# Kernel optimization log

Hardware: AMD Instinct MI355X
Metric: run time of the kernel (lower is better)

The kernel has to match this reference:

```python
import jax, jax.numpy as jnp
import numpy as np

EPS = 1e-4
SILU_GAIN = 1.0 / 0.596  # magnitude-preserving SiLU gain
SCALES = (4, 4, 8)       # prod == A_DIM == 128
T = 0.3                  # residual lerp weight


def mp_silu(x):
    return jax.nn.silu(x) * SILU_GAIN


def pixel_norm(x):
    # normalize over channel dim (axis=1) to unit RMS
    return x * jax.lax.rsqrt(jnp.mean(jnp.square(x), axis=1, keepdims=True) + EPS)


def norm_w(w):
    # magnitude-preserving conv: per-output-filter L2-normalized weight
    n = jnp.sqrt(jnp.sum(jnp.square(w), axis=tuple(range(1, w.ndim)), keepdims=True) + 1e-8)
    return w / n


def mp_add(a, b, t=T):
    return (a * (1.0 - t) + b * t) / np.sqrt((1.0 - t) ** 2 + t ** 2)


def conv2d(x, w, groups=1, padding=((0, 0), (0, 0))):
    return jax.lax.conv_general_dilated(
        x, w, (1, 1), padding,
        dimension_numbers=('NCHW', 'OIHW', 'NCHW'), feature_group_count=groups)


def conv1d(x, w, groups=1, padding=((0, 0),)):
    return jax.lax.conv_general_dilated(
        x, w, (1,), padding,
        dimension_numbers=('NCH', 'OIH', 'NCH'), feature_group_count=groups)


def avgpool_freq(x, s):
    B, C, F, L = x.shape
    return jnp.mean(x.reshape(B, C, F // s, s, L), axis=3)


def min_gru(h, w):
    # minGRU: z_t = sigmoid(Wz h_t), c_t = Wc h_t, s_t = (1-z_t) s_{t-1} + z_t c_t
    z, c = jnp.split(conv1d(h, norm_w(w)), 2, axis=1)
    z = jax.nn.sigmoid(z)
    a, b = 1.0 - z, z * c  # linear recurrence s_t = a_t s_{t-1} + b_t

    def comb(x, y):
        a1, b1 = x
        a2, b2 = y
        return a2 * a1, a2 * b1 + b2

    _, out = jax.lax.associative_scan(comb, (a, b), axis=-1)
    return out


def conv_block(x, w1, wd, w2, wdn, s):
    # x: [B, d, F, L]
    x = pixel_norm(x)
    r = mp_silu(x)
    r = conv2d(r, norm_w(w1))                                            # d -> h, 1x1
    r = conv2d(r, norm_w(wd), groups=wd.shape[0], padding=((2, 2), (1, 1)))  # depthwise 5x3
    r = mp_silu(r)
    r = conv2d(r, norm_w(w2))                                            # h -> d, 1x1
    h = mp_add(x, r)
    return conv2d(avgpool_freq(h, s), norm_w(wdn))                       # d -> 2d, freq /s


def seq_block(x, hg_w, dw_w, gru_w, out_w):
    # x: [B, d, L]
    x = pixel_norm(x)
    h, g = jnp.split(conv1d(x, norm_w(hg_w)), 2, axis=1)  # each [B, H, L]
    h = mp_silu(h)
    h = conv1d(h, norm_w(dw_w), groups=dw_w.shape[0], padding=((1, 1),))  # depthwise k=3
    h = mp_silu(h)
    h = min_gru(h, gru_w)
    h = h * mp_silu(g)
    return mp_add(x, conv1d(h, norm_w(out_w)))


def setup_inputs() -> dict:
    key = jax.random.key(0)
    ks = jax.random.split(key, 18)
    rn = lambda k, s: jax.random.normal(k, s, dtype=jnp.float32)
    B, L, A = 2, 2048, 128
    return {
        'audio': rn(ks[0], (B, A, L)),
        'proj_w': rn(ks[1], (64, 1, 1, 1)) * 0.5,
        'proj_b': jnp.zeros((64,), jnp.float32),
        'c0_w1': rn(ks[2], (128, 64, 1, 1)),
        'c0_wd': rn(ks[3], (128, 1, 5, 3)),
        'c0_w2': rn(ks[4], (64, 128, 1, 1)),
        'c0_dn': rn(ks[5], (128, 64, 1, 1)),
        'c1_w1': rn(ks[6], (256, 128, 1, 1)),
        'c1_wd': rn(ks[7], (256, 1, 5, 3)),
        'c1_w2': rn(ks[8], (128, 256, 1, 1)),
        'c1_dn': rn(ks[9], (256, 128, 1, 1)),
        'c2_w1': rn(ks[10], (512, 256, 1, 1)),
        'c2_wd': rn(ks[11], (512, 1, 5, 3)),
        'c2_w2': rn(ks[12], (256, 512, 1, 1)),
        'c2_dn': rn(ks[13], (512, 256, 1, 1)),
        'hg_w': rn(ks[14], (4, 2048, 512, 1)),
        'dw_w': rn(ks[15], (4, 1024, 1, 3)),
        'gru_w': rn(ks[16], (4, 2048, 1024, 1)),
        'out_w': rn(ks[17], (4, 512, 1024, 1)),
    }


def reference(audio, proj_w, proj_b,
              c0_w1, c0_wd, c0_w2, c0_dn,
              c1_w1, c1_wd, c1_w2, c1_dn,
              c2_w1, c2_wd, c2_w2, c2_dn,
              hg_w, dw_w, gru_w, out_w):
    h = audio[:, None]  # [B, 1, A_DIM, L]
    h = conv2d(h, proj_w) + proj_b[None, :, None, None]
    blocks = ((c0_w1, c0_wd, c0_w2, c0_dn),
              (c1_w1, c1_wd, c1_w2, c1_dn),
              (c2_w1, c2_wd, c2_w2, c2_dn))
    for (w1, wd, w2, dn), s in zip(blocks, SCALES):
        h = conv_block(h, w1, wd, w2, dn, s)
    h = h[:, :, 0, :]  # freq dim reduced to 1 -> [B, dim, L]
    for i in range(hg_w.shape[0]):
        h = seq_block(h, hg_w[i], dw_w[i], gru_w[i], out_w[i])
    return mp_silu(h)
```

## Files before the change

### kernel.cpp

```cpp
#include <hip/hip_runtime.h>
#include <math.h>

#define GAIN 1.6778523489932886f
#define MPS  1.3130643285972254f

typedef __attribute__((ext_vector_type(8))) short short8;
typedef __attribute__((ext_vector_type(4))) short short4v;
typedef __attribute__((ext_vector_type(4))) float float4v;

__device__ __forceinline__ float silu_g(float x){
  float s = 1.0f/(1.0f + __expf(-x));
  return x*s*GAIN;
}
__device__ __forceinline__ short f2bf(float f){
  unsigned u = __builtin_bit_cast(unsigned, f);
  u += 0x7fffu + ((u >> 16) & 1u);
  return (short)(u >> 16);
}
__device__ __forceinline__ float bf2f(unsigned short h){
  return __builtin_bit_cast(float, ((unsigned)h) << 16);
}

typedef __attribute__((address_space(3))) unsigned int as3_uint;
typedef const __attribute__((address_space(1))) unsigned int as1_cuint;
__device__ __forceinline__ void gload16(const unsigned short* gsrc, unsigned short* ldst){
  __builtin_amdgcn_global_load_lds((as1_cuint*)gsrc, (as3_uint*)ldst, 16, 0, 0);
}

struct NcEnt { const float* w; int O, K, dstOff; };
struct NcArgs { NcEnt e[16]; };

__global__ __launch_bounds__(64) void normcast_kernel(NcArgs na, unsigned short* __restrict__ wbf){
  int row = blockIdx.x;
  int base = 0; int i;
  for (i = 0; i < 16; i++){
    if (row < base + na.e[i].O) break;
    base += na.e[i].O;
  }
  if (i >= 16) return;
  int r = row - base; int K = na.e[i].K;
  const float* w = na.e[i].w + (long)r*K;
  unsigned short* dst = wbf + na.e[i].dstOff + (long)r*K;
  int tid = threadIdx.x;
  float s = 0.f;
  const bool v4 = ((K & 3) == 0);
  if (v4){
    for (int k = tid*4; k < K; k += 256){
      float4v v = *(const float4v*)&w[k];
      s += v[0]*v[0] + v[1]*v[1] + v[2]*v[2] + v[3]*v[3];
    }
  } else {
    for (int k = tid; k < K; k += 64){ float v = w[k]; s += v*v; }
  }
  for (int off = 32; off; off >>= 1) s += __shfl_down(s, off);
  float inv = rsqrtf(__shfl(s, 0) + 1e-8f);
  if (v4){
    for (int k = tid*4; k < K; k += 256){
      float4v v = *(const float4v*)&w[k];
      short4v o = { f2bf(v[0]*inv), f2bf(v[1]*inv), f2bf(v[2]*inv), f2bf(v[3]*inv) };
      *(short4v*)&dst[k] = o;
    }
  } else {
    for (int k = tid; k < K; k += 64) dst[k] = (unsigned short)f2bf(w[k]*inv);
  }
}

__global__ __launch_bounds__(64) void projstats_kernel(const float* __restrict__ pw, const float* __restrict__ pb,
                                                       float* __restrict__ S){
  int t = threadIdx.x;
  float p = pw[t], q = pb[t];
  float s1 = p*p, s2 = p*q, s3 = q*q;
  for (int off = 32; off; off >>= 1){
    s1 += __shfl_down(s1, off); s2 += __shfl_down(s2, off); s3 += __shfl_down(s3, off);
  }
  if (t == 0){ S[0] = s1; S[1] = s2; S[2] = s3; }
}

__global__ __launch_bounds__(256) void invn_audio_kernel(const float* __restrict__ audio, const float* __restrict__ S,
                                                         float* __restrict__ invn){
  long i = blockIdx.x*256 + threadIdx.x;
  if (i >= (2L*128*2048)/4) return;
  long e = i*4;
  float S1 = S[0], S2 = S[1], S3 = S[2];
  float4v a = *(const float4v*)&audio[e];
  float4v o;
  #pragma unroll
  for (int j = 0; j < 4; j++) o[j] = rsqrtf((a[j]*a[j]*S1 + 2.f*a[j]*S2 + S3)/64.f + 1e-4f);
  *(float4v*)&invn[e] = o;
}

template<int G, bool BF>
__global__ __launch_bounds__(256) void invn_reduce_kernel(const void* __restrict__ Xv, float* __restrict__ invn,
                                                          int C, int F){
  constexpr int L = 256/G;
  int t = threadIdx.x; int cs = t / L; int li = t % L;
  long pos = (long)blockIdx.x*L + li;
  int bf = (int)(pos >> 11); int l = (int)(pos & 2047);
  int b = bf / F; int f = bf - b*F;
  long base = ((long)b*C*F + f)*2048 + l;
  long stride = (long)F*2048;
  float s = 0.f;
  if (BF){
    const unsigned short* X = (const unsigned short*)Xv;
    for (int c = cs; c < C; c += G){ float v = bf2f(X[base + (long)c*stride]); s += v*v; }
  } else {
    const float* X = (const float*)Xv;
    for (int c = cs; c < C; c += G){ float v = X[base + (long)c*stride]; s += v*v; }
  }
  __shared__ float red[256];
  red[t] = s; __syncthreads();
  #pragma unroll
  for (int off = G/2; off > 0; off >>= 1){
    if (cs < off) red[t] += red[t + off*L];
    __syncthreads();
  }
  if (cs == 0) invn[pos] = rsqrtf(red[li]/(float)C + 1e-4f);
}

template<bool SILU, bool BF>
__global__ __launch_bounds__(256) void applynorm_kernel(const void* __restrict__ Xv, const float* __restrict__ invn,
                                                        unsigned short* __restrict__ XB, int C, int F, long total4){
  long i = blockIdx.x*256 + threadIdx.x;
  if (i >= total4) return;
  long e = i*4;
  int l = (int)(e & 2047); long r = e >> 11;
  int f = (int)(r % F); long bc = r / F; int b = (int)(bc / C);
  float4v x;
  if (BF){
    short4v u = *(const short4v*)((const unsigned short*)Xv + e);
    x = (float4v){ bf2f((unsigned short)u[0]), bf2f((unsigned short)u[1]),
                   bf2f((unsigned short)u[2]), bf2f((unsigned short)u[3]) };
  } else {
    x = *(const float4v*)((const float*)Xv + e);
  }
  float4v iv = *(const float4v*)&invn[((long)b*F + f)*2048 + l];
  short4v o;
  #pragma unroll
  for (int j = 0; j < 4; j++){
    float v = x[j]*iv[j];
    o[j] = f2bf(SILU ? silu_g(v) : v);
  }
  *(short4v*)&XB[e] = o;
}

__global__ __launch_bounds__(256) void normT_kernel(const float* __restrict__ SEQ,
                                                    const float* __restrict__ invn,
                                                    unsigned short* __restrict__ XST){
  __shared__ float tile[64][65];
  const int l0 = blockIdx.x*64, c0 = blockIdx.y*64, b = blockIdx.z;
  const int t = threadIdx.x;
  const int lr = (t & 15)*4;
  const int cr = t >> 4;
  #pragma unroll
  for (int p = 0; p < 4; p++){
    int c = cr + p*16;
    float4v v = *(const float4v*)&SEQ[((long)(b*512 + c0 + c))*2048 + l0 + lr];
    tile[c][lr+0] = v[0]; tile[c][lr+1] = v[1]; tile[c][lr+2] = v[2]; tile[c][lr+3] = v[3];
  }
  __syncthreads();
  const int cc = (t & 7)*8;
  const int lw = t >> 3;
  #pragma unroll
  for (int p = 0; p < 2; p++){
    int l = lw + p*32;
    float iv = invn[b*2048 + l0 + l];
    short8 o;
    #pragma unroll
    for (int j = 0; j < 8; j++) o[j] = f2bf(tile[cc+j][l] * iv);
    *(short8*)&XST[((long)(b*2048 + l0 + l))*512 + c0 + cc] = o;
  }
}

struct GTArgs {
  const unsigned short* A;
  const unsigned short* B;
  unsigned short* O1;
  unsigned short* O2;
  int N, K;
};

template<int EMODE>
__global__ __launch_bounds__(256,2) void gemmT_kernel(GTArgs g){
  __shared__ __align__(16) char SMEMraw[49152];
  unsigned short (*Asm)[4096] = (unsigned short (*)[4096])SMEMraw;
  unsigned short (*Bsm)[4096] = (unsigned short (*)[4096])(SMEMraw + 24576);
  const int t = threadIdx.x;
  const int lane = t & 63;
  const int wc = (t >> 7) & 1;
  const int wsd = (t >> 6) & 1;
  const int q = lane >> 4, r16 = lane & 15;
  const int m0 = blockIdx.x * 128;
  const int n0 = blockIdx.y * 128;
  const int K = g.K;

  const int r0 = t >> 2;
  const int c8 = (((t & 3) ^ ((r0 >> 1) & 3)) << 3);
  const unsigned short* Ap = g.A + (long)(n0 + r0)*K + c8;
  const unsigned short* Bp = g.B + (long)(m0 + r0)*K + c8;

  auto stage = [&](int bi, int k0){
    gload16(Ap + k0,           &Asm[bi][t*8]);
    gload16(Ap + 64*K + k0,    &Asm[bi][2048 + t*8]);
    gload16(Bp + k0,           &Bsm[bi][t*8]);
    gload16(Bp + 64*K + k0,    &Bsm[bi][2048 + t*8]);
  };

  float4v acc[4][4];
  #pragma unroll
  for (int i = 0; i < 4; i++)
    #pragma unroll
    for (int j = 0; j < 4; j++) acc[i][j] = (float4v){0.f,0.f,0.f,0.f};

  const int nit = K >> 5;
  stage(0, 0);
  stage(1, 32);

  const int qsw = ((q ^ ((r16 >> 1) & 3)) << 3);

  for (int it = 0; it < nit; ++it){
    if (it + 2 < nit){
      stage((it + 2) % 3, (it + 2) << 5);
      asm volatile("" ::: "memory");
      asm volatile("s_waitcnt vmcnt(8)" ::: "memory");
    } else if (it + 1 < nit){
      asm volatile("s_waitcnt vmcnt(4)" ::: "memory");
    } else {
      asm volatile("s_waitcnt vmcnt(0)" ::: "memory");
    }
    __builtin_amdgcn_s_barrier();
    asm volatile("" ::: "memory");

    const unsigned short* As = Asm[it % 3];
    const unsigned short* Bs = Bsm[it % 3];
    short8 afr[4], bfr[4];
    #pragma unroll
    for (int i = 0; i < 4; i++) afr[i] = *(const short8*)&As[(wc*64 + i*16 + r16)*32 + qsw];
    #pragma unroll
    for (int j = 0; j < 4; j++) bfr[j] = *(const short8*)&Bs[(wsd*64 + j*16 + r16)*32 + qsw];
    #pragma unroll
    for (int i = 0; i < 4; i++)
      #pragma unroll
      for (int j = 0; j < 4; j++)
        acc[i][j] = __builtin_amdgcn_mfma_f32_16x16x32_bf16(afr[i], bfr[j], acc[i][j], 0, 0, 0);

    asm volatile("" ::: "memory");
    __builtin_amdgcn_s_barrier();
  }

  if (EMODE == 1 && n0 < 1024){
    float* Cf = (float*)SMEMraw;
    #pragma unroll
    for (int h = 0; h < 2; h++){
      __syncthreads();
      if (wc == h){
        #pragma unroll
        for (int j = 0; j < 4; j++){
          int m = wsd*64 + j*16 + r16;
          #pragma unroll
          for (int i = 0; i < 4; i++)
            *(float4v*)&Cf[m*68 + i*16 + q*4] = acc[i][j];
        }
      }
      __syncthreads();
      #pragma unroll
      for (int p = 0; p < 4; p++){
        int m = (t >> 3) + p*32;
        int n8 = (t & 7)*8;
        int gm = m0 + m; int b = gm >> 11, l = gm & 2047;
        float4v v0 = *(const float4v*)&Cf[m*68 + n8];
        float4v v1 = *(const float4v*)&Cf[m*68 + n8 + 4];
        short8 o;
        #pragma unroll
        for (int e = 0; e < 4; e++){ o[e] = f2bf(silu_g(v0[e])); o[e+4] = f2bf(silu_g(v1[e])); }
        *(short8*)&g.O1[((long)(b*2048 + l))*1024 + (n0 + h*64 + n8)] = o;
      }
    }
  } else {
    float* Csm = (float*)SMEMraw;
    #pragma unroll
    for (int qtr = 0; qtr < 4; qtr++){
      __syncthreads();
      if (wc == (qtr >> 1)){
        #pragma unroll
        for (int ii = 0; ii < 2; ii++){
          int i = (qtr & 1)*2 + ii;
          #pragma unroll
          for (int j = 0; j < 4; j++){
            int m = wsd*64 + j*16 + r16;
            #pragma unroll
            for (int rg = 0; rg < 4; rg++)
              Csm[(ii*16 + q*4 + rg)*132 + m] = acc[i][j][rg];
          }
        }
      }
      __syncthreads();
      #pragma unroll
      for (int sp = 0; sp < 2; sp++){
        int nrow = (t >> 4) + sp*16;
        int n = n0 + qtr*32 + nrow;
        int m8 = (t & 15)*8;
        int gm = m0 + m8; int b = gm >> 11, l = gm & 2047;
        float4v v0 = *(const float4v*)&Csm[nrow*132 + m8];
        float4v v1 = *(const float4v*)&Csm[nrow*132 + m8 + 4];
        short8 o;
        #pragma unroll
        for (int e = 0; e < 4; e++){ o[e] = f2bf(v0[e]); o[e+4] = f2bf(v1[e]); }
        if (EMODE == 1) *(short8*)&g.O2[((long)(b*1024 + (n - 1024)))*2048 + l] = o;
        else            *(short8*)&g.O1[((long)(b*2048 + n))*2048 + l] = o;
      }
    }
  }
}

struct GemmArgs {
  const unsigned short* A;
  const unsigned short* Bh;
  const float* invn; const float* audio;
  const float* pw; const float* pb;
  const unsigned short* auxXH;
  unsigned short* CoutH; unsigned short* Cout2H;
  int N, K, Fdim, Lw, lq0, BLw, Bl0, CLw, Cl0, Nsto, Fsrc;
};

template<int BMODE, int EMODE>
__global__ __launch_bounds__(256,2) void mgemm_kernel(GemmArgs g){
  __shared__ __align__(16) char SMEMraw[20480];
  unsigned short* Asm = (unsigned short*)SMEMraw;
  unsigned short* Bsm = Asm + 128*40;
  const int t = threadIdx.x;
  const int lane = t & 63;
  const int wave = t >> 6;
  const int wc = wave >> 1, wsd = wave & 1;
  const int q = lane >> 4, r16 = lane & 15;
  const int s0 = blockIdx.x * 128;
  const int n0 = blockIdx.y * 128;
  const int FL = g.Fdim * g.Lw;

  const int ar = t >> 1, ah = t & 1;
  const int an = n0 + ar;
  const bool aval = an < g.N;
  const unsigned short* Aptr = g.A + (long)an*g.K + ah*16;

  const int kg = t & 7, mg = t >> 3;
  const int mb = s0 + mg*4;
  int bcol = mb / FL; int rr = mb - bcol*FL;
  int fcol = (g.Fdim > 1) ? (rr / g.Lw) : 0;
  int labs = g.lq0 + (rr - fcol*g.Lw);
  const bool cv = (bcol < 2);
  bool lv[4];
  #pragma unroll
  for (int j = 0; j < 4; j++) lv[j] = cv && (labs + j >= 0) && (labs + j < 2048);
  const bool vec4 = cv && (labs >= 0) && (labs + 3 < 2048);
  const unsigned short* bbase = g.Bh;
  if (cv) bbase = g.Bh + ((long)(bcol*g.K)*g.Fsrc + fcol)*g.BLw + (labs - g.Bl0);
  const long kstep = (long)g.Fsrc * g.BLw;

  float invn4[4] = {0,0,0,0}, aud4[4] = {0,0,0,0};
  if (BMODE == 2){
    #pragma unroll
    for (int j = 0; j < 4; j++) if (lv[j]){
      invn4[j] = g.invn[(bcol*g.Fdim + fcol)*2048 + labs + j];
      aud4[j]  = g.audio[(bcol*128 + fcol)*2048 + labs + j];
    }
  }

  float4v acc[4][4];
  #pragma unroll
  for (int i = 0; i < 4; i++)
    #pragma unroll
    for (int j = 0; j < 4; j++) acc[i][j] = (float4v){0.f,0.f,0.f,0.f};

  short8 pa0 = {0,0,0,0,0,0,0,0}, pa1 = {0,0,0,0,0,0,0,0};
  short4v praw[4];
  #pragma unroll
  for (int i = 0; i < 4; i++) praw[i] = (short4v){0,0,0,0};

  auto ldA = [&](int kb){
    if (aval){
      pa0 = *(const short8*)(Aptr + kb);
      pa1 = *(const short8*)(Aptr + kb + 8);
    }
  };
  auto ldB = [&](int kb){
    #pragma unroll
    for (int i = 0; i < 4; i++){
      const int k = kb + kg*4 + i;
      const unsigned short* bp = bbase + (long)k*kstep;
      if (vec4) praw[i] = *(const short4v*)bp;
      else {
        short4v u = {0,0,0,0};
        #pragma unroll
        for (int j = 0; j < 4; j++) if (lv[j]) u[j] = (short)bp[j];
        praw[i] = u;
      }
    }
  };

  ldA(0);
  if (BMODE == 0) ldB(0);

  for (int k0 = 0; k0 < g.K; k0 += 32){
    short8 sa0 = pa0, sa1 = pa1;
    short4v bpk[4];
    if (BMODE == 0){
      #pragma unroll
      for (int j = 0; j < 4; j++){
        short4v p;
        #pragma unroll
        for (int i = 0; i < 4; i++) p[i] = praw[i][j];
        bpk[j] = p;
      }
    } else {
      float tv[4][4];
      #pragma unroll
      for (int i = 0; i < 4; i++){
        const int k = k0 + kg*4 + i;
        const float pwk = g.pw[k], pbk = g.pb[k];
        #pragma unroll
        for (int j = 0; j < 4; j++) tv[i][j] = lv[j] ? silu_g((aud4[j]*pwk + pbk)*invn4[j]) : 0.f;
      }
      #pragma unroll
      for (int j = 0; j < 4; j++){
        short4v p;
        #pragma unroll
        for (int i = 0; i < 4; i++) p[i] = f2bf(tv[i][j]);
        bpk[j] = p;
      }
    }
    if (k0 + 32 < g.K){
      ldA(k0 + 32);
      if (BMODE == 0) ldB(k0 + 32);
    }

    __syncthreads();
    *(short8*)&Asm[ar*40 + ah*16]     = sa0;
    *(short8*)&Asm[ar*40 + ah*16 + 8] = sa1;
    #pragma unroll
    for (int j = 0; j < 4; j++)
      *(short4v*)&Bsm[(mg*4 + j)*40 + kg*4] = bpk[j];
    __syncthreads();

    short8 afr[4], bfr[4];
    #pragma unroll
    for (int i = 0; i < 4; i++) afr[i] = *(const short8*)&Asm[(wc*64 + i*16 + r16)*40 + q*8];
    #pragma unroll
    for (int j = 0; j < 4; j++) bfr[j] = *(const short8*)&Bsm[(wsd*64 + j*16 + r16)*40 + q*8];
    #pragma unroll
    for (int i = 0; i < 4; i++)
      #pragma unroll
      for (int j = 0; j < 4; j++)
        acc[i][j] = __builtin_amdgcn_mfma_f32_16x16x32_bf16(afr[i], bfr[j], acc[i][j], 0, 0, 0);
  }

  {
    float* Csm = (float*)SMEMraw;
    #pragma unroll
    for (int qtr = 0; qtr < 4; qtr++){
      __syncthreads();
      if (wc == (qtr >> 1)){
        #pragma unroll
        for (int ii = 0; ii < 2; ii++){
          int i = (qtr & 1)*2 + ii;
          #pragma unroll
          for (int j = 0; j < 4; j++){
            int m = wsd*64 + j*16 + r16;
            #pragma unroll
            for (int rg = 0; rg < 4; rg++)
              Csm[(ii*16 + q*4 + rg)*132 + m] = acc[i][j][rg];
          }
        }
      }
      __syncthreads();
      #pragma unroll
      for (int sp = 0; sp < 2; sp++){
        int nrow = (t >> 4) + sp*16;
        int n = n0 + qtr*32 + nrow;
        int m8 = (t & 15)*8;
        if (n >= g.N) continue;
        int sg = s0 + m8;
        int b2 = sg / FL; int r2 = sg - b2*FL;
        if (b2 >= 2) continue;
        int f2 = (g.Fdim > 1) ? (r2 / g.Lw) : 0;
        int l2 = g.lq0 + (r2 - f2*g.Lw);
        float4v v0 = *(const float4v*)&Csm[nrow*132 + m8];
        float4v v1 = *(const float4v*)&Csm[nrow*132 + m8 + 4];
        long obase = ((long)(b2*g.Nsto + n)*g.Fdim + f2)*g.CLw + (l2 - g.Cl0);
        short8 o;
        if (EMODE == 1){
          #pragma unroll
          for (int e = 0; e < 4; e++){ o[e] = f2bf(v0[e]); o[e+4] = f2bf(v1[e]); }
        } else if (EMODE == 2){
          short8 axv = *(const short8*)&g.auxXH[((long)(b2*g.N + n)*g.Fdim + f2)*2048 + l2];
          const float* ivp = &g.invn[(b2*g.Fdim + f2)*2048 + l2];
          float4v iv0 = *(const float4v*)ivp;
          float4v iv1 = *(const float4v*)(ivp + 4);
          #pragma unroll
          for (int e = 0; e < 4; e++){
            float xn0 = bf2f((unsigned short)axv[e]) * iv0[e];
            float xn1 = bf2f((unsigned short)axv[e+4]) * iv1[e];
            o[e]   = f2bf((xn0*0.7f + v0[e]*0.3f)*MPS);
            o[e+4] = f2bf((xn1*0.7f + v1[e]*0.3f)*MPS);
          }
        } else {
          float pwn = g.pw[n], pbn = g.pb[n];
          const float* ap  = &g.audio[(b2*128 + f2)*2048 + l2];
          const float* ivp = &g.invn[(b2*g.Fdim + f2)*2048 + l2];
          float4v a0 = *(const float4v*)ap,  a1 = *(const float4v*)(ap + 4);
          float4v iv0 = *(const float4v*)ivp, iv1 = *(const float4v*)(ivp + 4);
          #pragma unroll
          for (int e = 0; e < 4; e++){
            float xn0 = (a0[e]*pwn + pbn)*iv0[e];
            float xn1 = (a1[e]*pwn + pbn)*iv1[e];
            o[e]   = f2bf((xn0*0.7f + v0[e]*0.3f)*MPS);
            o[e+4] = f2bf((xn1*0.7f + v1[e]*0.3f)*MPS);
          }
        }
        *(short8*)&g.CoutH[obase] = o;
      }
    }
  }
}

struct DnArgs {
  const unsigned short* A; const unsigned short* P;
  float* Cout; unsigned short* CoutH;
  int N, K, F2, Lc, l0;
};

template<int EMODE>
__global__ __launch_bounds__(256,4) void mgemm64_kernel(DnArgs g){
  __shared__ __align__(16) char SMEM[10240];
  unsigned short* Asm = (unsigned short*)SMEM;
  unsigned short* Bsm = Asm + 64*40;
  const int t = threadIdx.x;
  const int lane = t & 63;
  const int wave = t >> 6;
  const int wc = wave >> 1, wsd = wave & 1;
  const int q = lane >> 4, r16 = lane & 15;
  const int s0 = blockIdx.x * 64;
  const int n0 = blockIdx.y * 64;
  const int FL = g.F2 * g.Lc;

  const int ar = t >> 2, ah = t & 3;
  const unsigned short* Aptr = g.A + (long)(n0 + ar)*g.K + ah*8;
  const int kg = t & 7, mg = t >> 3;
  const bool bstage = (mg < 16);
  const int mb = s0 + (mg & 15)*4;
  const int bcol = mb / FL; const int rr = mb - bcol*FL;
  const int fcol = rr / g.Lc; const int li = rr - fcol*g.Lc;
  const unsigned short* bbase = g.P + ((long)(bcol*g.K)*g.F2 + fcol)*g.Lc + li;
  const long kstep = (long)g.F2 * g.Lc;

  float4v acc[2][2];
  #pragma unroll
  for (int i = 0; i < 2; i++)
    #pragma unroll
    for (int j = 0; j < 2; j++) acc[i][j] = (float4v){0.f,0.f,0.f,0.f};

  short8 pa = {0,0,0,0,0,0,0,0};
  short4v praw[4];
  #pragma unroll
  for (int i = 0; i < 4; i++) praw[i] = (short4v){0,0,0,0};

  auto ldA = [&](int kb){ pa = *(const short8*)(Aptr + kb); };
  auto ldB = [&](int kb){
    if (bstage){
      #pragma unroll
      for (int i = 0; i < 4; i++)
        praw[i] = *(const short4v*)(bbase + (long)(kb + kg*4 + i)*kstep);
    }
  };
  ldA(0); ldB(0);

  for (int k0 = 0; k0 < g.K; k0 += 32){
    short8 sa = pa;
    short4v bpk[4];
    #pragma unroll
    for (int j = 0; j < 4; j++){
      short4v p;
      #pragma unroll
      for (int i = 0; i < 4; i++) p[i] = praw[i][j];
      bpk[j] = p;
    }
    if (k0 + 32 < g.K){ ldA(k0 + 32); ldB(k0 + 32); }

    __syncthreads();
    *(short8*)&Asm[ar*40 + ah*8] = sa;
    if (bstage){
      #pragma unroll
      for (int j = 0; j < 4; j++)
        *(short4v*)&Bsm[((mg & 15)*4 + j)*40 + kg*4] = bpk[j];
    }
    __syncthreads();

    short8 afr[2], bfr[2];
    #pragma unroll
    for (int i = 0; i < 2; i++) afr[i] = *(const short8*)&Asm[(wc*32 + i*16 + r16)*40 + q*8];
    #pragma unroll
    for (int j = 0; j < 2; j++) bfr[j] = *(const short8*)&Bsm[(wsd*32 + j*16 + r16)*40 + q*8];
    #pragma unroll
    for (int i = 0; i < 2; i++)
      #pragma unroll
      for (int j = 0; j < 2; j++)
        acc[i][j] = __builtin_amdgcn_mfma_f32_16x16x32_bf16(afr[i], bfr[j], acc[i][j], 0, 0, 0);
  }

  {
    float* Csm = (float*)SMEM;
    const int b2 = s0 / FL; const int r20 = s0 - b2*FL;
    const int f2c = r20 / g.Lc; const int l2c = g.l0 + (r20 - f2c*g.Lc);
    #pragma unroll
    for (int nq = 0; nq < 4; nq++){
      __syncthreads();
      if (wc == (nq >> 1)){
        const int i = nq & 1;
        #pragma unroll
        for (int j = 0; j < 2; j++)
          #pragma unroll
          for (int rg = 0; rg < 4; rg++)
            Csm[(q*4 + rg)*68 + wsd*32 + j*16 + r16] = acc[i][j][rg];
      }
      __syncthreads();
      int nrow = t >> 4;
      int mq = (t & 15)*4;
      int n = n0 + nq*16 + nrow;
      float4v v = *(const float4v*)&Csm[nrow*68 + mq];
      long oidx = ((long)(b2*g.N + n)*g.F2 + f2c)*2048 + l2c + mq;
      if (EMODE == 0){
        *(float4v*)&g.Cout[oidx] = v;
      } else {
        short4v o = { f2bf(v[0]), f2bf(v[1]), f2bf(v[2]), f2bf(v[3]) };
        *(short4v*)&g.CoutH[oidx] = o;
      }
    }
  }
}

template<int EMODE>
__global__ __launch_bounds__(256,4) void seqout_kernel(const unsigned short* __restrict__ A,
                                                       const unsigned short* __restrict__ Bh,
                                                       const float* __restrict__ invn,
                                                       const float* __restrict__ auxX,
                                                       float* __restrict__ Cout, int K){
  __shared__ __align__(16) char SMEM[10240];
  unsigned short* Asm = (unsigned short*)SMEM;
  unsigned short* Bsm = Asm + 64*40;
  const int t = threadIdx.x;
  const int lane = t & 63;
  const int wave = t >> 6;
  const int wc = wave >> 1, wsd = wave & 1;
  const int q = lane >> 4, r16 = lane & 15;
  const int s0 = blockIdx.x * 64;
  const int n0 = blockIdx.y * 64;

  const int ar = t >> 2, ah = t & 3;
  const unsigned short* Aptr = A + (long)(n0 + ar)*K + ah*8;
  const int kg = t & 7, mg = t >> 3;
  const bool bstage = (mg < 16);
  const int mb = s0 + (mg & 15)*4;
  const int bcol = mb >> 11, lb = mb & 2047;
  const unsigned short* bbase = Bh + ((long)bcol*K)*2048 + lb;

  float4v acc[2][2];
  #pragma unroll
  for (int i = 0; i < 2; i++)
    #pragma unroll
    for (int j = 0; j < 2; j++) acc[i][j] = (float4v){0.f,0.f,0.f,0.f};

  short8 pa = {0,0,0,0,0,0,0,0};
  short4v praw[4];
  #pragma unroll
  for (int i = 0; i < 4; i++) praw[i] = (short4v){0,0,0,0};

  auto ldA = [&](int kb){ pa = *(const short8*)(Aptr + kb); };
  auto ldB = [&](int kb){
    if (bstage){
      #pragma unroll
      for (int i = 0; i < 4; i++)
        praw[i] = *(const short4v*)(bbase + (long)(kb + kg*4 + i)*2048);
    }
  };
  ldA(0); ldB(0);

  for (int k0 = 0; k0 < K; k0 += 32){
    short8 sa = pa;
    short4v bpk[4];
    #pragma unroll
    for (int j = 0; j < 4; j++){
      short4v p;
      #pragma unroll
      for (int i = 0; i < 4; i++) p[i] = praw[i][j];
      bpk[j] = p;
    }
    if (k0 + 32 < K){ ldA(k0 + 32); ldB(k0 + 32); }

    __syncthreads();
    *(short8*)&Asm[ar*40 + ah*8] = sa;
    if (bstage){
      #pragma unroll
      for (int j = 0; j < 4; j++)
        *(short4v*)&Bsm[((mg & 15)*4 + j)*40 + kg*4] = bpk[j];
    }
    __syncthreads();

    short8 afr[2], bfr[2];
    #pragma unroll
    for (int i = 0; i < 2; i++) afr[i] = *(const short8*)&Asm[(wc*32 + i*16 + r16)*40 + q*8];
    #pragma unroll
    for (int j = 0; j < 2; j++) bfr[j] = *(const short8*)&Bsm[(wsd*32 + j*16 + r16)*40 + q*8];
    #pragma unroll
    for (int i = 0; i < 2; i++)
      #pragma unroll
      for (int j = 0; j < 2; j++)
        acc[i][j] = __builtin_amdgcn_mfma_f32_16x16x32_bf16(afr[i], bfr[j], acc[i][j], 0, 0, 0);
  }

  {
    float* Csm = (float*)SMEM;
    const int b2 = s0 >> 11; const int l0b = s0 & 2047;
    #pragma unroll
    for (int nq = 0; nq < 4; nq++){
      __syncthreads();
      if (wc == (nq >> 1)){
        const int i = nq & 1;
        #pragma unroll
        for (int j = 0; j < 2; j++)
          #pragma unroll
          for (int rg = 0; rg < 4; rg++)
            Csm[(q*4 + rg)*68 + wsd*32 + j*16 + r16] = acc[i][j][rg];
      }
      __syncthreads();
      int nrow = t >> 4;
      int mq = (t & 15)*4;
      int n = n0 + nq*16 + nrow;
      int l = l0b + mq;
      float4v v = *(const float4v*)&Csm[nrow*68 + mq];
      float4v ax = *(const float4v*)&auxX[((long)b2*512 + n)*2048 + l];
      float4v iv = *(const float4v*)&invn[b2*2048 + l];
      float4v r;
      #pragma unroll
      for (int e = 0; e < 4; e++){
        float xn = ax[e]*iv[e];
        float rr = (xn*0.7f + v[e]*0.3f)*MPS;
        r[e] = (EMODE == 6) ? silu_g(rr) : rr;
      }
      *(float4v*)&Cout[((long)b2*512 + n)*2048 + l] = r;
    }
  }
}

__global__ __launch_bounds__(256) void poolf_kernel(const unsigned short* __restrict__ Hb,
                                                    unsigned short* __restrict__ P,
                                                    int F2, int s, int Lc, long total4){
  long i = blockIdx.x*256 + threadIdx.x;
  if (i >= total4) return;
  long e = i*4;
  int li = (int)(e % Lc); long r0 = e / Lc;
  int f2 = (int)(r0 % F2); long r = r0 / F2;
  const unsigned short* src = Hb + ((long)r*F2*s + (long)f2*s)*Lc + li;
  float a0=0,a1=0,a2=0,a3=0;
  for (int p = 0; p < s; p++){
    short4v u = *(const short4v*)(src + (long)p*Lc);
    a0 += bf2f((unsigned short)u[0]); a1 += bf2f((unsigned short)u[1]);
    a2 += bf2f((unsigned short)u[2]); a3 += bf2f((unsigned short)u[3]);
  }
  float inv = 1.f/(float)s;
  short4v o = { f2bf(a0*inv), f2bf(a1*inv), f2bf(a2*inv), f2bf(a3*inv) };
  *(short4v*)&P[((long)r*F2 + f2)*Lc + li] = o;
}

struct DwArgs { const unsigned short* R1; const unsigned short* wd; unsigned short* R2; int C, F, Lc, l0; };
__global__ __launch_bounds__(256) void dw2d_kernel(DwArgs a){
  int idx = blockIdx.x*256 + threadIdx.x;
  int Lq = a.Lc >> 3;
  int Fq = a.F >> 3;
  int total = 2*a.C*Fq*Lq;
  if (idx >= total) return;
  int lq = idx % Lq; int r = idx / Lq;
  int fq = r % Fq; r /= Fq;
  int c = r % a.C; int b = r / a.C;
  int f0 = fq*8;
  int labs = a.l0 + lq*8;
  int Lw = a.Lc + 8;
  const unsigned short* base = a.R1 + (long)((b*a.C + c)*a.F)*Lw + (labs - (a.l0 - 4));
  const unsigned short* w = a.wd + c*15;
  float W[5][3];
  #pragma unroll
  for (int tp = 0; tp < 5; tp++)
    #pragma unroll
    for (int j = 0; j < 3; j++) W[tp][j] = bf2f(w[tp*3 + j]);

  const bool llo = (labs > 0);
  const bool lhi = (labs + 8 < 2048);
  float acc[8][8];
  #pragma unroll
  for (int t = 0; t < 8; t++)
    #pragma unroll
    for (int j = 0; j < 8; j++) acc[t][j] = 0.f;

  #pragma unroll
  for (int r12 = 0; r12 < 12; r12++){
    int rrow = f0 - 2 + r12;
    if (rrow < 0 || rrow >= a.F) continue;
    const unsigned short* p = base + (long)rrow*Lw;
    short4v u0 = *(const short4v*)p;
    short4v u1 = *(const short4v*)(p + 4);
    float x[10];
    x[0] = llo ? bf2f(p[-1]) : 0.f;
    x[1] = bf2f((unsigned short)u0[0]); x[2] = bf2f((unsigned short)u0[1]);
    x[3] = bf2f((unsigned short)u0[2]); x[4] = bf2f((unsigned short)u0[3]);
    x[5] = bf2f((unsigned short)u1[0]); x[6] = bf2f((unsigned short)u1[1]);
    x[7] = bf2f((unsigned short)u1[2]); x[8] = bf2f((unsigned short)u1[3]);
    x[9] = lhi ? bf2f(p[8]) : 0.f;
    #pragma unroll
    for (int t = 0; t < 8; t++){
      const int df = r12 - 2 - t;
      if (df < -2 || df > 2) continue;
      float w0 = W[df+2][0], w1 = W[df+2][1], w2 = W[df+2][2];
      #pragma unroll
      for (int j = 0; j < 8; j++)
        acc[t][j] += w0*x[j] + w1*x[j+1] + w2*x[j+2];
    }
  }

  unsigned short* ob = a.R2 + ((long)((b*a.C + c)*a.F + f0))*a.Lc + (labs - a.l0);
  #pragma unroll
  for (int t = 0; t < 8; t++){
    short8 o;
    #pragma unroll
    for (int j = 0; j < 8; j++) o[j] = f2bf(silu_g(acc[t][j]));
    *(short8*)(ob + (long)t*a.Lc) = o;
  }
}

__global__ __launch_bounds__(256) void dwseqT_kernel(const unsigned short* __restrict__ HST,
                                                     const unsigned short* __restrict__ w,
                                                     unsigned short* __restrict__ H2T){
  int idx = blockIdx.x*256 + threadIdx.x;
  if (idx >= 2*2048*128) return;
  int c0 = (idx & 127) * 8; long bt = idx >> 7;
  int tt = (int)(bt & 2047);
  const unsigned short* base = HST + bt*1024 + c0;
  short8 zz = {0,0,0,0,0,0,0,0};
  short8 x1 = *(const short8*)base;
  short8 x0 = (tt > 0)    ? *(const short8*)(base - 1024) : zz;
  short8 x2 = (tt < 2047) ? *(const short8*)(base + 1024) : zz;
  const unsigned short* wp = w + c0*3;
  short8 o;
  #pragma unroll
  for (int j = 0; j < 8; j++){
    float w0 = bf2f(wp[3*j]), w1 = bf2f(wp[3*j+1]), w2 = bf2f(wp[3*j+2]);
    float v = w0*bf2f((unsigned short)x0[j]) + w1*bf2f((unsigned short)x1[j]) + w2*bf2f((unsigned short)x2[j]);
    o[j] = f2bf(silu_g(v));
  }
  *(short8*)&H2T[bt*1024 + c0] = o;
}

__global__ __launch_bounds__(256) void scan_kernel(const unsigned short* __restrict__ ZC, const unsigned short* __restrict__ G,
                                                   unsigned short* __restrict__ SC){
  int bc = blockIdx.x;
  int b = bc >> 10, c = bc & 1023;
  const unsigned short* zrow = ZC + ((long)(b*2048 + c))*2048;
  const unsigned short* crow = ZC + ((long)(b*2048 + 1024 + c))*2048;
  const unsigned short* grow = G + (long)bc*2048;
  unsigned short* orow = SC + (long)bc*2048;
  int tid = threadIdx.x;
  int t0 = tid*8;
  short8 zv = *(const short8*)&zrow[t0];
  short8 cv = *(const short8*)&crow[t0];
  float av[8], bv[8];
  float A = 1.f, Bv = 0.f;
  #pragma unroll
  for (int j = 0; j < 8; j++){
    float z = bf2f((unsigned short)zv[j]); float cval = bf2f((unsigned short)cv[j]);
    float zs = 1.f/(1.f + __expf(-z));
    float a = 1.f - zs; float bb = zs*cval;
    av[j] = a; bv[j] = bb;
    Bv = a*Bv + bb;
    A = a*A;
  }
  __shared__ float sA[256], sB[256];
  sA[tid] = A; sB[tid] = Bv;
  __syncthreads();
  for (int off = 1; off < 256; off <<= 1){
    float pA = 1.f, pB = 0.f;
    if (tid >= off){ pA = sA[tid-off]; pB = sB[tid-off]; }
    __syncthreads();
    float nA = A*pA; float nB = A*pB + Bv;
    A = nA; Bv = nB;
    sA[tid] = A; sB[tid] = Bv;
    __syncthreads();
  }
  float h = (tid > 0) ? sB[tid-1] : 0.f;
  short8 gv = *(const short8*)&grow[t0];
  short8 ov;
  #pragma unroll
  for (int j = 0; j < 8; j++){
    h = av[j]*h + bv[j];
    ov[j] = f2bf(h * silu_g(bf2f((unsigned short)gv[j])));
  }
  *(short8*)&orow[t0] = ov;
}

extern "C" void kernel_launch(void* const* d_in, const int* in_sizes, int n_in,
                              void* d_out, int out_size, void* d_ws, size_t ws_size,
                              hipStream_t stream) {
  const float* audio = (const float*)d_in[0];
  const float* pw = (const float*)d_in[1];
  const float* pb = (const float*)d_in[2];
  const float* cw1[3] = {(const float*)d_in[3], (const float*)d_in[7], (const float*)d_in[11]};
  const float* cwd[3] = {(const float*)d_in[4], (const float*)d_in[8], (const float*)d_in[12]};
  const float* cw2[3] = {(const float*)d_in[5], (const float*)d_in[9], (const float*)d_in[13]};
  const float* cdn[3] = {(const float*)d_in[6], (const float*)d_in[10], (const float*)d_in[14]};
  const float* hgw  = (const float*)d_in[15];
  const float* dww  = (const float*)d_in[16];
  const float* gruw = (const float*)d_in[17];
  const float* outw = (const float*)d_in[18];
  float* out = (float*)d_out;

  char* P0 = (char*)d_ws;
  float*          INVW = (float*)P0;                    P0 += 131072;
  unsigned short* WBF  = (unsigned short*)P0;           P0 += 30443776;
  float*          INVN = (float*)P0;                    P0 += 2097152;
  char*           XBZC = P0;                            P0 += 33554432;
  unsigned short* IN1h = (unsigned short*)P0;           P0 += 33554432;
  unsigned short* IN2h = (unsigned short*)P0;           P0 += 16777216;
  float*          SEQ  = (float*)P0;                    P0 += 8388608;
  char*           ARENA = P0;
  long arenaBytes = (long)ws_size - (long)(P0 - (char*)d_ws);
  float* S = INVW + 32000;

  const float* wsrc[16] = {cw1[0],cwd[0],cw2[0],cdn[0], cw1[1],cwd[1],cw2[1],cdn[1],
                           cw1[2],cwd[2],cw2[2],cdn[2], hgw, dww, gruw, outw};
  int Os[16] = {128,128,64,128, 256,256,128,256, 512,512,256,512, 8192,4096,8192,2048};
  int Ks[16] = {64,15,128,64, 128,15,256,128, 256,15,512,256, 512,3,1024,1024};
  int wbfOff[16];
  {
    int wo = 0;
    for (int i = 0; i < 16; i++){ wbfOff[i] = wo; wo += Os[i]*Ks[i]; }
  }
  {
    NcArgs na;
    int rows = 0;
    for (int i = 0; i < 16; i++){
      na.e[i].w = wsrc[i]; na.e[i].O = Os[i]; na.e[i].K = Ks[i]; na.e[i].dstOff = wbfOff[i];
      rows += Os[i];
    }
    normcast_kernel<<<rows, 64, 0, stream>>>(na, WBF);
  }
  projstats_kernel<<<1, 64, 0, stream>>>(pw, pb, S);

  int Cin_[3]  = {64,128,256};
  int Cmid_[3] = {128,256,512};
  int F_[3]    = {128,32,8};
  int s_[3]    = {4,4,8};
  const unsigned short* XinH[3] = {nullptr, IN1h, IN2h};
  unsigned short* XoutH[3] = {IN1h, IN2h, nullptr};
  int iW1[3]={0,4,8}, iWd[3]={1,5,9}, iW2[3]={2,6,10}, iDn[3]={3,7,11};

  for (int b = 0; b < 3; b++){
    int Cin = Cin_[b], Cmid = Cmid_[b], F = F_[b], s = s_[b];
    int F2 = F/s;
    int nc = 16;
    for (int c = 1; c <= 16; c <<= 1){
      long Lc = 2048/c;
      long bytes = 2L*(2L*Cmid*F*(Lc+8) + 2L*Cmid*F*Lc + 2L*Cin*F*Lc + 2L*Cin*F2*Lc);
      if (bytes <= arenaBytes){ nc = c; break; }
    }
    int Lc = 2048/nc;
    unsigned short* R1 = (unsigned short*)ARENA;
    unsigned short* R2 = R1 + 2L*Cmid*F*(Lc+8);
    unsigned short* Hb = R2 + 2L*Cmid*F*Lc;
    unsigned short* Pb = Hb + 2L*Cin*F*Lc;
    unsigned short* XB = (unsigned short*)XBZC;

    if (b == 0){
      invn_audio_kernel<<<(2*128*2048/4+255)/256, 256, 0, stream>>>(audio, S, INVN);
    } else {
      int positions = 2*F*2048;
      invn_reduce_kernel<8,true><<<positions/32, 256, 0, stream>>>(XinH[b], INVN, Cin, F);
      long total4 = (long)2*Cin*F*2048/4;
      applynorm_kernel<true,true><<<(int)((total4+255)/256), 256, 0, stream>>>(XinH[b], INVN, XB, Cin, F, total4);
    }

    for (int ci = 0; ci < nc; ci++){
      int l0 = ci*Lc;
      GemmArgs ga{};
      ga.A = WBF + wbfOff[iW1[b]];
      ga.Bh = XB; ga.invn = INVN; ga.audio = audio; ga.pw = pw; ga.pb = pb;
      ga.CoutH = R1; ga.N = Cmid; ga.K = Cin; ga.Fdim = F; ga.Lw = Lc+8; ga.lq0 = l0-4;
      ga.BLw = 2048; ga.Bl0 = 0; ga.CLw = Lc+8; ga.Cl0 = l0-4; ga.Nsto = Cmid; ga.Fsrc = F;
      int M1 = 2*F*(Lc+8);
      dim3 g1((M1+127)/128, (Cmid+127)/128);
      if (b == 0) mgemm_kernel<2,1><<<g1,256,0,stream>>>(ga);
      else        mgemm_kernel<0,1><<<g1,256,0,stream>>>(ga);
      DwArgs da{R1, WBF + wbfOff[iWd[b]], R2, Cmid, F, Lc, l0};
      int tdw = 2*Cmid*(F/8)*(Lc/8);
      dw2d_kernel<<<(tdw+255)/256, 256, 0, stream>>>(da);
      GemmArgs gb{};
      gb.A = WBF + wbfOff[iW2[b]];
      gb.Bh = R2; gb.invn = INVN; gb.audio = audio; gb.pw = pw; gb.pb = pb; gb.auxXH = XinH[b];
      gb.CoutH = Hb; gb.N = Cin; gb.K = Cmid; gb.Fdim = F; gb.Lw = Lc; gb.lq0 = l0;
      gb.BLw = Lc; gb.Bl0 = l0; gb.CLw = Lc; gb.Cl0 = l0; gb.Nsto = Cin; gb.Fsrc = F;
      int M2 = 2*F*Lc;
      dim3 g2((M2+127)/128, (Cin+127)/128);
      if (b == 0) mgemm_kernel<0,3><<<g2,256,0,stream>>>(gb);
      else        mgemm_kernel<0,2><<<g2,256,0,stream>>>(gb);
      long tp4 = (2L*Cin*F2*Lc)/4;
      poolf_kernel<<<(int)((tp4+255)/256), 256, 0, stream>>>(Hb, Pb, F2, s, Lc, tp4);
      DnArgs dn{};
      dn.A = WBF + wbfOff[iDn[b]]; dn.P = Pb;
      dn.Cout = SEQ; dn.CoutH = XoutH[b];
      dn.N = Cmid; dn.K = Cin; dn.F2 = F2; dn.Lc = Lc; dn.l0 = l0;
      dim3 gdn((2*F2*Lc)/64, Cmid/64);
      if (b == 2) mgemm64_kernel<0><<<gdn,256,0,stream>>>(dn);
      else        mgemm64_kernel<1><<<gdn,256,0,stream>>>(dn);
    }
  }

  unsigned short* XST = IN1h;
  unsigned short* HST = XST + 2097152;
  unsigned short* G   = HST + 4194304;
  unsigned short* H2T = G  + 4194304;
  unsigned short* SC  = H2T + 4194304;
  unsigned short* ZCh = (unsigned short*)XBZC;

  for (int i = 0; i < 4; i++){
    invn_reduce_kernel<16,false><<<4096/16, 256, 0, stream>>>(SEQ, INVN, 512, 1);
    normT_kernel<<<dim3(32,8,2), 256, 0, stream>>>(SEQ, INVN, XST);
    GTArgs gh{ WBF + wbfOff[12] + (long)i*2048*512, XST, HST, G, 2048, 512 };
    gemmT_kernel<1><<<dim3(32,16), 256, 0, stream>>>(gh);
    dwseqT_kernel<<<2048, 256, 0, stream>>>(HST, WBF + wbfOff[13] + i*1024*3, H2T);
    GTArgs gz{ WBF + wbfOff[14] + (long)i*2048*1024, H2T, ZCh, nullptr, 2048, 1024 };
    gemmT_kernel<0><<<dim3(32,16), 256, 0, stream>>>(gz);
    scan_kernel<<<2048,256,0,stream>>>(ZCh, G, SC);
    const unsigned short* oA = WBF + wbfOff[15] + (long)i*512*1024;
    if (i < 3) seqout_kernel<5><<<dim3(64,8),256,0,stream>>>(oA, SC, INVN, SEQ, SEQ, 1024);
    else       seqout_kernel<6><<<dim3(64,8),256,0,stream>>>(oA, SC, INVN, SEQ, out, 1024);
  }

  (void)in_sizes; (void)n_in; (void)out_size;
}
```

Measured before the change: 1.216 ms.

## Halve depthwise conv row tile and use wavefront-shuffle scan in minGRU

The depthwise 5x3 conv kernel now has each thread compute 4 frequency rows instead of 8. This doubles the thread count and cuts the accumulator registers, at the cost of more redundant halo row loads (8 loaded rows per 4 outputs instead of 12 per 8). The minGRU block scan swaps its shared-memory Hillis-Steele loop, which needed many __syncthreads, for an intra-wavefront __shfl_up scan plus a small cross-wave combine through shared memory with a single barrier. This assumes a 64-wide wavefront and a fixed 256-thread block.

```diff
diff --git a/kernel.cpp b/kernel.cpp
--- a/kernel.cpp
+++ b/kernel.cpp
@@ -773,13 +773,13 @@
 __global__ __launch_bounds__(256) void dw2d_kernel(DwArgs a){
   int idx = blockIdx.x*256 + threadIdx.x;
   int Lq = a.Lc >> 3;
-  int Fq = a.F >> 3;
+  int Fq = a.F >> 2;
   int total = 2*a.C*Fq*Lq;
   if (idx >= total) return;
   int lq = idx % Lq; int r = idx / Lq;
   int fq = r % Fq; r /= Fq;
   int c = r % a.C; int b = r / a.C;
-  int f0 = fq*8;
+  int f0 = fq*4;
   int labs = a.l0 + lq*8;
   int Lw = a.Lc + 8;
   const unsigned short* base = a.R1 + (long)((b*a.C + c)*a.F)*Lw + (labs - (a.l0 - 4));
@@ -792,15 +792,15 @@
 
   const bool llo = (labs > 0);
   const bool lhi = (labs + 8 < 2048);
-  float acc[8][8];
-  #pragma unroll
-  for (int t = 0; t < 8; t++)
+  float acc[4][8];
+  #pragma unroll
+  for (int t = 0; t < 4; t++)
     #pragma unroll
     for (int j = 0; j < 8; j++) acc[t][j] = 0.f;
 
   #pragma unroll
-  for (int r12 = 0; r12 < 12; r12++){
-    int rrow = f0 - 2 + r12;
+  for (int r8 = 0; r8 < 8; r8++){
+    int rrow = f0 - 2 + r8;
     if (rrow < 0 || rrow >= a.F) continue;
     const unsigned short* p = base + (long)rrow*Lw;
     short4v u0 = *(const short4v*)p;
@@ -813,8 +813,8 @@
     x[7] = bf2f((unsigned short)u1[2]); x[8] = bf2f((unsigned short)u1[3]);
     x[9] = lhi ? bf2f(p[8]) : 0.f;
     #pragma unroll
-    for (int t = 0; t < 8; t++){
-      const int df = r12 - 2 - t;
+    for (int t = 0; t < 4; t++){
+      const int df = r8 - 2 - t;
       if (df < -2 || df > 2) continue;
       float w0 = W[df+2][0], w1 = W[df+2][1], w2 = W[df+2][2];
       #pragma unroll
@@ -825,7 +825,7 @@
 
   unsigned short* ob = a.R2 + ((long)((b*a.C + c)*a.F + f0))*a.Lc + (labs - a.l0);
   #pragma unroll
-  for (int t = 0; t < 8; t++){
+  for (int t = 0; t < 4; t++){
     short8 o;
     #pragma unroll
     for (int j = 0; j < 8; j++) o[j] = f2bf(silu_g(acc[t][j]));
@@ -879,19 +879,26 @@
     Bv = a*Bv + bb;
     A = a*A;
   }
-  __shared__ float sA[256], sB[256];
-  sA[tid] = A; sB[tid] = Bv;
+  int lane = tid & 63, wv = tid >> 6;
+  float iA = A, iB = Bv;
+  #pragma unroll
+  for (int off = 1; off < 64; off <<= 1){
+    float pA = __shfl_up(iA, off);
+    float pB = __shfl_up(iB, off);
+    if (lane >= off){ iB = iA*pB + iB; iA = iA*pA; }
+  }
+  float exA = __shfl_up(iA, 1);
+  float exB = __shfl_up(iB, 1);
+  if (lane == 0){ exA = 1.f; exB = 0.f; }
+  __shared__ float sWA[4], sWB[4];
+  if (lane == 63){ sWA[wv] = iA; sWB[wv] = iB; }
   __syncthreads();
-  for (int off = 1; off < 256; off <<= 1){
-    float pA = 1.f, pB = 0.f;
-    if (tid >= off){ pA = sA[tid-off]; pB = sB[tid-off]; }
-    __syncthreads();
-    float nA = A*pA; float nB = A*pB + Bv;
-    A = nA; Bv = nB;
-    sA[tid] = A; sB[tid] = Bv;
-    __syncthreads();
-  }
-  float h = (tid > 0) ? sB[tid-1] : 0.f;
+  float wpA = 1.f, wpB = 0.f;
+  #pragma unroll
+  for (int w = 0; w < 3; w++){
+    if (w < wv){ wpB = sWA[w]*wpB + sWB[w]; wpA = wpA*sWA[w]; }
+  }
+  float h = exA*wpB + exB;
   short8 gv = *(const short8*)&grow[t0];
   short8 ov;
   #pragma unroll
@@ -995,7 +1002,7 @@
       if (b == 0) mgemm_kernel<2,1><<<g1,256,0,stream>>>(ga);
       else        mgemm_kernel<0,1><<<g1,256,0,stream>>>(ga);
       DwArgs da{R1, WBF + wbfOff[iWd[b]], R2, Cmid, F, Lc, l0};
-      int tdw = 2*Cmid*(F/8)*(Lc/8);
+      int tdw = 2*Cmid*(F/4)*(Lc/8);
       dw2d_kernel<<<(tdw+255)/256, 256, 0, stream>>>(da);
       GemmArgs gb{};
       gb.A = WBF + wbfOff[iW2[b]];
```

Result: faster. 1.107 ms (-8.9%).
